# Optimization experiments

Hardware: AMD Instinct MI355X
Metric: run time of the kernel (lower is better)

## Reference

```python
import jax, jax.numpy as jnp
import numpy as np

N_NODES = 50000
N_EDGES = 800000
N_GRAPHS = 64
IN_DIM, HID, MLP_HID, NUM_CLASSES = 384, 128, 64, 1


def setup_inputs() -> dict:
    key = jax.random.key(0)
    ks = jax.random.split(key, 10)
    x = jax.random.normal(ks[0], (N_NODES, IN_DIM), jnp.float32)
    edge_index = jax.random.randint(ks[1], (2, N_EDGES), 0, N_NODES, dtype=jnp.int32)
    batch = jnp.sort(jax.random.randint(ks[2], (N_NODES,), 0, N_GRAPHS, dtype=jnp.int32))

    def glorot(k, shape):
        fan_in = shape[0]
        return jax.random.normal(k, shape, jnp.float32) / jnp.sqrt(jnp.float32(fan_in))

    return {
        "x": x,
        "edge_index": edge_index,
        "batch": batch,
        "W1": glorot(ks[3], (IN_DIM, HID)),  "b1": jnp.zeros((HID,), jnp.float32),
        "W2": glorot(ks[4], (HID, HID)),     "b2": jnp.zeros((HID,), jnp.float32),
        "W3": glorot(ks[5], (HID, HID)),     "b3": jnp.zeros((HID,), jnp.float32),
        "Wm1": glorot(ks[6], (HID, MLP_HID)), "bm1": jnp.zeros((MLP_HID,), jnp.float32),
        "Wm2": glorot(ks[7], (MLP_HID, NUM_CLASSES)), "bm2": jnp.zeros((NUM_CLASSES,), jnp.float32),
    }


def _gcn_conv(x, W, b, src, dst, dis):
    # PyG GCNConv: h = x W; aggregate D^-1/2 (A+I) D^-1/2 h; add bias.
    n = x.shape[0]
    h = x @ W                               # [N, out]
    enorm = dis[src] * dis[dst]             # [E] symmetric normalization
    msgs = h[src] * enorm[:, None]          # gather + scale
    agg = jax.ops.segment_sum(msgs, dst, num_segments=n)
    agg = agg + h * (dis * dis)[:, None]    # self-loop contribution
    return agg + b


def reference(x, edge_index, batch, W1, b1, W2, b2, W3, b3, Wm1, bm1, Wm2, bm2):
    src, dst = edge_index[0], edge_index[1]
    n = x.shape[0]
    # degree over A + I (self-loops added, as in PyG gcn_norm)
    deg = jax.ops.segment_sum(jnp.ones((src.shape[0],), x.dtype), dst, num_segments=n) + 1.0
    dis = jax.lax.rsqrt(deg)

    h = jax.nn.relu(_gcn_conv(x, W1, b1, src, dst, dis))
    h = jax.nn.relu(_gcn_conv(h, W2, b2, src, dst, dis))
    h = jax.nn.relu(_gcn_conv(h, W3, b3, src, dst, dis))

    # global mean pool over graphs
    counts = jax.ops.segment_sum(jnp.ones((n,), x.dtype), batch, num_segments=N_GRAPHS)
    pooled = jax.ops.segment_sum(h, batch, num_segments=N_GRAPHS)
    pooled = pooled / jnp.maximum(counts, 1.0)[:, None]   # [G, HID]

    # MLP head (dropout = identity in eval mode)
    z = jax.nn.relu(pooled @ Wm1 + bm1)
    out = z @ Wm2 + bm2                                    # [G, 1]
    return out
```

## Files before the change

kernel.cpp:

```cpp
#include <hip/hip_runtime.h>
#include <hip/hip_bf16.h>

#define N_NODES 50000
#define N_EDGES 800000
#define N_GRAPHS 64
#define IN_DIM 384
#define HID 128
#define MLP_HID 64

#define SCAN_BLOCKS ((N_NODES + 255) / 256)
#define POOL_CHUNK 128
#define POOL_BLOCKS ((N_NODES + POOL_CHUNK - 1) / POOL_CHUNK)
#define GEMM_BLOCKS ((N_NODES + 127) / 128)

typedef __attribute__((ext_vector_type(8))) short short8;
typedef __attribute__((ext_vector_type(4))) float f32x4;
typedef unsigned int u32;

__global__ __launch_bounds__(256) void count_kernel(const int* __restrict__ dst,
                                                    int* __restrict__ cnt, int E) {
    int t = blockIdx.x * 256 + threadIdx.x;
    if (t < E) atomicAdd(&cnt[dst[t]], 1);
}

__global__ __launch_bounds__(256) void bsum_kernel(const int* __restrict__ cnt,
                                                   int* __restrict__ bsum) {
    __shared__ int sh[256];
    const int t = threadIdx.x;
    const int i = blockIdx.x * 256 + t;
    sh[t] = (i < N_NODES) ? cnt[i] : 0;
    __syncthreads();
#pragma unroll
    for (int off = 128; off > 0; off >>= 1) {
        if (t < off) sh[t] += sh[t + off];
        __syncthreads();
    }
    if (t == 0) bsum[blockIdx.x] = sh[0];
}

__global__ __launch_bounds__(256) void bscan_kernel(const int* __restrict__ bsum,
                                                    int* __restrict__ boff,
                                                    int* __restrict__ rowptr) {
    __shared__ int sh[256];
    const int t = threadIdx.x;
    int v = (t < SCAN_BLOCKS) ? bsum[t] : 0;
    sh[t] = v;
    __syncthreads();
#pragma unroll
    for (int off = 1; off < 256; off <<= 1) {
        int u = 0;
        if (t >= off) u = sh[t - off];
        __syncthreads();
        if (t >= off) sh[t] += u;
        __syncthreads();
    }
    if (t < SCAN_BLOCKS) boff[t] = sh[t] - v;
    if (t == 255) rowptr[N_NODES] = sh[255];
}

__global__ __launch_bounds__(256) void final_scan_kernel(const int* __restrict__ cnt,
                                                         const int* __restrict__ boff,
                                                         int* __restrict__ rowptr,
                                                         int* __restrict__ cursor,
                                                         float* __restrict__ dis) {
    __shared__ int sh[256];
    const int t = threadIdx.x;
    const int i = blockIdx.x * 256 + t;
    const int c = (i < N_NODES) ? cnt[i] : 0;
    sh[t] = c;
    __syncthreads();
#pragma unroll
    for (int off = 1; off < 256; off <<= 1) {
        int u = 0;
        if (t >= off) u = sh[t - off];
        __syncthreads();
        if (t >= off) sh[t] += u;
        __syncthreads();
    }
    if (i < N_NODES) {
        const int pos = boff[blockIdx.x] + sh[t] - c;
        rowptr[i] = pos;
        cursor[i] = pos;
        dis[i] = rsqrtf((float)c + 1.0f);
    }
}

__global__ __launch_bounds__(256) void fill_kernel(const int* __restrict__ ei,
                                                   int* __restrict__ cursor,
                                                   int* __restrict__ csr, int E) {
    int e = blockIdx.x * 256 + threadIdx.x;
    if (e >= E) return;
    int s = ei[e];
    int d = ei[E + e];
    int pos = atomicAdd(&cursor[d], 1);
    csr[pos] = s;
}

__global__ __launch_bounds__(256) void wsplit_kernel(const float* __restrict__ W,
                                                     ushort* __restrict__ hi,
                                                     ushort* __restrict__ lo, int K) {
    int t = blockIdx.x * 256 + threadIdx.x;
    if (t >= K * 128) return;
    const int k = t >> 7;
    const int c = t & 127;
    const float f = W[t];
    const u32 u = __float_as_uint(f);
    const u32 h = u & 0xFFFF0000u;
    const float lf = f - __uint_as_float(h);
    hi[c * K + k] = (ushort)(u >> 16);
    lo[c * K + k] = (ushort)(__float_as_uint(lf) >> 16);
}

template <int K, bool RELU_IN>
__global__ __launch_bounds__(256) void gemm_mfma_kernel(const float* __restrict__ X,
                                                        const ushort* __restrict__ Wthi,
                                                        const ushort* __restrict__ Wtlo,
                                                        float* __restrict__ H, int M) {
    __shared__ ushort Ahi[128][40];
    __shared__ ushort Alo[128][40];
    __shared__ ushort Bhi[128][40];
    __shared__ ushort Blo[128][40];

    const int tid = threadIdx.x;
    const int row0 = blockIdx.x * 128;

    const int srow = tid >> 1;
    const int skq  = (tid & 1) << 4;

    const int lane = tid & 63;
    const int wave = tid >> 6;
    const int wr = (wave >> 1) * 64;
    const int wc = (wave & 1) * 64;
    const int li = lane & 15;
    const int kb = (lane >> 4) << 3;

    f32x4 acc[4][4];
#pragma unroll
    for (int m = 0; m < 4; ++m)
#pragma unroll
        for (int n = 0; n < 4; ++n) acc[m][n] = (f32x4){0.f, 0.f, 0.f, 0.f};

    for (int k0 = 0; k0 < K; k0 += 32) {
        {
            const int gr = row0 + srow;
            const float* src = &X[(size_t)(gr < M ? gr : (M - 1)) * K + k0 + skq];
            float f[16];
            *reinterpret_cast<float4*>(f)      = *reinterpret_cast<const float4*>(src);
            *reinterpret_cast<float4*>(f + 4)  = *reinterpret_cast<const float4*>(src + 4);
            *reinterpret_cast<float4*>(f + 8)  = *reinterpret_cast<const float4*>(src + 8);
            *reinterpret_cast<float4*>(f + 12) = *reinterpret_cast<const float4*>(src + 12);
            u32 hp[8], lp[8];
#pragma unroll
            for (int i = 0; i < 8; ++i) {
                float f0 = f[2 * i], f1 = f[2 * i + 1];
                if (RELU_IN) { f0 = fmaxf(f0, 0.f); f1 = fmaxf(f1, 0.f); }
                const u32 u0 = __float_as_uint(f0), u1 = __float_as_uint(f1);
                const u32 h0 = u0 & 0xFFFF0000u, h1 = u1 & 0xFFFF0000u;
                const float l0 = f0 - __uint_as_float(h0);
                const float l1 = f1 - __uint_as_float(h1);
                hp[i] = (h0 >> 16) | h1;
                lp[i] = (__float_as_uint(l0) >> 16) | (__float_as_uint(l1) & 0xFFFF0000u);
            }
            u32* dh = (u32*)&Ahi[srow][skq];
            u32* dl = (u32*)&Alo[srow][skq];
            *reinterpret_cast<uint4*>(dh)     = make_uint4(hp[0], hp[1], hp[2], hp[3]);
            *reinterpret_cast<uint4*>(dh + 4) = make_uint4(hp[4], hp[5], hp[6], hp[7]);
            *reinterpret_cast<uint4*>(dl)     = make_uint4(lp[0], lp[1], lp[2], lp[3]);
            *reinterpret_cast<uint4*>(dl + 4) = make_uint4(lp[4], lp[5], lp[6], lp[7]);
        }
        {
            const ushort* sh = &Wthi[srow * K + k0 + skq];
            const ushort* sl = &Wtlo[srow * K + k0 + skq];
            *reinterpret_cast<uint4*>(&Bhi[srow][skq])     = *reinterpret_cast<const uint4*>(sh);
            *reinterpret_cast<uint4*>(&Bhi[srow][skq + 8]) = *reinterpret_cast<const uint4*>(sh + 8);
            *reinterpret_cast<uint4*>(&Blo[srow][skq])     = *reinterpret_cast<const uint4*>(sl);
            *reinterpret_cast<uint4*>(&Blo[srow][skq + 8]) = *reinterpret_cast<const uint4*>(sl + 8);
        }
        __syncthreads();
        short8 ah[4], al[4];
#pragma unroll
        for (int m = 0; m < 4; ++m) {
            ah[m] = *reinterpret_cast<const short8*>(&Ahi[wr + m * 16 + li][kb]);
            al[m] = *reinterpret_cast<const short8*>(&Alo[wr + m * 16 + li][kb]);
        }
#pragma unroll
        for (int n = 0; n < 4; ++n) {
            const short8 bh = *reinterpret_cast<const short8*>(&Bhi[wc + n * 16 + li][kb]);
            const short8 bl = *reinterpret_cast<const short8*>(&Blo[wc + n * 16 + li][kb]);
#pragma unroll
            for (int m = 0; m < 4; ++m) {
                acc[m][n] = __builtin_amdgcn_mfma_f32_16x16x32_bf16(ah[m], bh, acc[m][n], 0, 0, 0);
                acc[m][n] = __builtin_amdgcn_mfma_f32_16x16x32_bf16(ah[m], bl, acc[m][n], 0, 0, 0);
                acc[m][n] = __builtin_amdgcn_mfma_f32_16x16x32_bf16(al[m], bh, acc[m][n], 0, 0, 0);
            }
        }
        __syncthreads();
    }
    const int rbase = (lane >> 4) << 2;
#pragma unroll
    for (int m = 0; m < 4; ++m) {
        const int gr0 = row0 + wr + m * 16 + rbase;
#pragma unroll
        for (int r = 0; r < 4; ++r) {
            const int grow = gr0 + r;
            if (grow < M) {
#pragma unroll
                for (int n = 0; n < 4; ++n) {
                    H[(size_t)grow * 128 + wc + n * 16 + li] = acc[m][n][r];
                }
            }
        }
    }
}

__global__ __launch_bounds__(256) void gather_kernel(const int* __restrict__ rowptr,
                                                     const int* __restrict__ csr,
                                                     const float* __restrict__ H,
                                                     const float* __restrict__ dis,
                                                     const float* __restrict__ b,
                                                     float* __restrict__ AGG, int n) {
    int t = blockIdx.x * 256 + threadIdx.x;
    int node = t >> 5;
    if (node >= n) return;
    int lane = t & 31;
    const int beg = rowptr[node];
    const int end = rowptr[node + 1];
    const float d = dis[node];

    float4 acc;
    {
        float4 h = *reinterpret_cast<const float4*>(&H[node * 128 + lane * 4]);
        float4 bb = *reinterpret_cast<const float4*>(&b[lane * 4]);
        const float dd = d * d;
        acc.x = fmaf(h.x, dd, bb.x);
        acc.y = fmaf(h.y, dd, bb.y);
        acc.z = fmaf(h.z, dd, bb.z);
        acc.w = fmaf(h.w, dd, bb.w);
    }
    int i = beg;
    for (; i + 2 <= end; i += 2) {
        const int s0 = csr[i];
        const int s1 = csr[i + 1];
        const float e0 = dis[s0] * d;
        const float e1 = dis[s1] * d;
        float4 v0 = *reinterpret_cast<const float4*>(&H[s0 * 128 + lane * 4]);
        float4 v1 = *reinterpret_cast<const float4*>(&H[s1 * 128 + lane * 4]);
        acc.x = fmaf(v0.x, e0, acc.x);
        acc.y = fmaf(v0.y, e0, acc.y);
        acc.z = fmaf(v0.z, e0, acc.z);
        acc.w = fmaf(v0.w, e0, acc.w);
        acc.x = fmaf(v1.x, e1, acc.x);
        acc.y = fmaf(v1.y, e1, acc.y);
        acc.z = fmaf(v1.z, e1, acc.z);
        acc.w = fmaf(v1.w, e1, acc.w);
    }
    if (i < end) {
        const int s0 = csr[i];
        const float e0 = dis[s0] * d;
        float4 v0 = *reinterpret_cast<const float4*>(&H[s0 * 128 + lane * 4]);
        acc.x = fmaf(v0.x, e0, acc.x);
        acc.y = fmaf(v0.y, e0, acc.y);
        acc.z = fmaf(v0.z, e0, acc.z);
        acc.w = fmaf(v0.w, e0, acc.w);
    }
    *reinterpret_cast<float4*>(&AGG[node * 128 + lane * 4]) = acc;
}

__global__ __launch_bounds__(256) void pool1_kernel(const float* __restrict__ AGG,
                                                    const int* __restrict__ batch,
                                                    float* __restrict__ pooled, int n) {
    const int start = blockIdx.x * POOL_CHUNK;
    const int end = min(start + POOL_CHUNK, n);
    const int f = threadIdx.x & 127;
    const int h = threadIdx.x >> 7;
    int gcur = -1;
    float acc = 0.f;
    for (int i = start + h; i < end; i += 2) {
        const int g = batch[i];
        if (g != gcur) {
            if (gcur >= 0) atomicAdd(&pooled[gcur * HID + f], acc);
            gcur = g;
            acc = 0.f;
        }
        acc += fmaxf(AGG[i * HID + f], 0.f);
    }
    if (gcur >= 0) atomicAdd(&pooled[gcur * HID + f], acc);
}

__global__ __launch_bounds__(128) void pooldiv_kernel(const int* __restrict__ batch,
                                                      float* __restrict__ pooled, int n) {
    const int g = blockIdx.x;
    int lo = 0, hi = n;
    while (lo < hi) { int mid = (lo + hi) >> 1; if (batch[mid] < g) lo = mid + 1; else hi = mid; }
    const int start = lo;
    hi = n;
    while (lo < hi) { int mid = (lo + hi) >> 1; if (batch[mid] < g + 1) lo = mid + 1; else hi = mid; }
    const float cnt = (float)(lo - start);
    pooled[g * HID + threadIdx.x] /= fmaxf(cnt, 1.f);
}

__global__ __launch_bounds__(256) void mlp_kernel(const float* __restrict__ pooled,
                                                  const float* __restrict__ Wm1,
                                                  const float* __restrict__ bm1,
                                                  const float* __restrict__ Wm2,
                                                  const float* __restrict__ bm2,
                                                  float* __restrict__ out) {
    __shared__ float P[N_GRAPHS][HID];
    __shared__ float Wl[HID][MLP_HID];
    const int tid = threadIdx.x;
    for (int i = tid; i < N_GRAPHS * HID; i += 256) P[i >> 7][i & 127] = pooled[i];
    for (int i = tid; i < HID * MLP_HID; i += 256) Wl[i >> 6][i & 63] = Wm1[i];
    __syncthreads();
    const int g = tid >> 2;
    const int jb = tid & 3;
    float part = 0.f;
#pragma unroll
    for (int jj = 0; jj < 16; ++jj) {
        const int j = jb * 16 + jj;
        float z = bm1[j];
        for (int k = 0; k < HID; ++k) z = fmaf(P[g][k], Wl[k][j], z);
        z = fmaxf(z, 0.f);
        part = fmaf(z, Wm2[j], part);
    }
    part += __shfl_xor(part, 1);
    part += __shfl_xor(part, 2);
    if (jb == 0) out[g] = part + bm2[0];
}

extern "C" void kernel_launch(void* const* d_in, const int* in_sizes, int n_in,
                              void* d_out, int out_size, void* d_ws, size_t ws_size,
                              hipStream_t stream) {
    const float* x   = (const float*)d_in[0];
    const int*   ei  = (const int*)d_in[1];
    const int*   bat = (const int*)d_in[2];
    const float* W1  = (const float*)d_in[3];
    const float* b1  = (const float*)d_in[4];
    const float* W2  = (const float*)d_in[5];
    const float* b2  = (const float*)d_in[6];
    const float* W3  = (const float*)d_in[7];
    const float* b3  = (const float*)d_in[8];
    const float* Wm1 = (const float*)d_in[9];
    const float* bm1 = (const float*)d_in[10];
    const float* Wm2 = (const float*)d_in[11];
    const float* bm2 = (const float*)d_in[12];
    float* out = (float*)d_out;

    int*   cnt    = (int*)d_ws;
    int*   cursor = cnt + 50048;
    int*   rowptr = cursor + 50048;
    int*   csr    = rowptr + 50056;
    int*   bsum   = csr + 800000;
    int*   boff   = bsum + 256;
    float* dis    = (float*)(boff + 256);
    float* H      = dis + 50048;
    float* AGG    = H + N_NODES * HID;
    float* pooled = AGG + N_NODES * HID;
    ushort* wt1hi = (ushort*)(pooled + 8192);
    ushort* wt1lo = wt1hi + IN_DIM * HID;
    ushort* wt2hi = wt1lo + IN_DIM * HID;
    ushort* wt2lo = wt2hi + HID * HID;
    ushort* wt3hi = wt2lo + HID * HID;
    ushort* wt3lo = wt3hi + HID * HID;

    hipMemsetAsync(cnt, 0, N_NODES * sizeof(int), stream);
    hipMemsetAsync(pooled, 0, N_GRAPHS * HID * sizeof(float), stream);

    count_kernel<<<(N_EDGES + 255) / 256, 256, 0, stream>>>(ei + N_EDGES, cnt, N_EDGES);
    bsum_kernel<<<SCAN_BLOCKS, 256, 0, stream>>>(cnt, bsum);
    bscan_kernel<<<1, 256, 0, stream>>>(bsum, boff, rowptr);
    final_scan_kernel<<<SCAN_BLOCKS, 256, 0, stream>>>(cnt, boff, rowptr, cursor, dis);
    fill_kernel<<<(N_EDGES + 255) / 256, 256, 0, stream>>>(ei, cursor, csr, N_EDGES);

    wsplit_kernel<<<(IN_DIM * HID + 255) / 256, 256, 0, stream>>>(W1, wt1hi, wt1lo, IN_DIM);
    wsplit_kernel<<<(HID * HID + 255) / 256, 256, 0, stream>>>(W2, wt2hi, wt2lo, HID);
    wsplit_kernel<<<(HID * HID + 255) / 256, 256, 0, stream>>>(W3, wt3hi, wt3lo, HID);

    const int gat_blocks = (N_NODES * 32 + 255) / 256;

    gemm_mfma_kernel<IN_DIM, false><<<GEMM_BLOCKS, 256, 0, stream>>>(x, wt1hi, wt1lo, H, N_NODES);
    gather_kernel<<<gat_blocks, 256, 0, stream>>>(rowptr, csr, H, dis, b1, AGG, N_NODES);
    gemm_mfma_kernel<HID, true><<<GEMM_BLOCKS, 256, 0, stream>>>(AGG, wt2hi, wt2lo, H, N_NODES);
    gather_kernel<<<gat_blocks, 256, 0, stream>>>(rowptr, csr, H, dis, b2, AGG, N_NODES);
    gemm_mfma_kernel<HID, true><<<GEMM_BLOCKS, 256, 0, stream>>>(AGG, W3 ? wt3hi : wt3hi, wt3lo, H, N_NODES);
    gather_kernel<<<gat_blocks, 256, 0, stream>>>(rowptr, csr, H, dis, b3, AGG, N_NODES);

    pool1_kernel<<<POOL_BLOCKS, 256, 0, stream>>>(AGG, bat, pooled, N_NODES);
    pooldiv_kernel<<<N_GRAPHS, 128, 0, stream>>>(bat, pooled, N_NODES);
    mlp_kernel<<<1, 256, 0, stream>>>(pooled, Wm1, bm1, Wm2, bm2, out);
}
```

Baseline: 537.7 us.

## Pre-scale GEMM output by dis, simplify gather, fuse pooling, merge wsplits

The GEMM epilogue now multiplies each output row by its dis value. This lets the gather drop the per-edge dis[src] load and its multiply and apply the destination scale once at the end. The gather switches to one 64-lane wavefront per node with float2 loads and 4-way unrolling. The last layer's gather fuses ReLU and mean-pool accumulation through shared memory and atomics, which removes the separate pool kernel and one full pass over AGG. The three weight-split launches are merged into one kernel; the cost is an extra dis load in the GEMM and more atomics when a block spans graph boundaries.

```diff
diff --git a/kernel.cpp b/kernel.cpp
--- a/kernel.cpp
+++ b/kernel.cpp
@@ -9,9 +9,8 @@
 #define MLP_HID 64
 
 #define SCAN_BLOCKS ((N_NODES + 255) / 256)
-#define POOL_CHUNK 128
-#define POOL_BLOCKS ((N_NODES + POOL_CHUNK - 1) / POOL_CHUNK)
 #define GEMM_BLOCKS ((N_NODES + 127) / 128)
+#define GATHER_BLOCKS (N_NODES / 4)
 
 typedef __attribute__((ext_vector_type(8))) short short8;
 typedef __attribute__((ext_vector_type(4))) float f32x4;
@@ -96,11 +95,8 @@
     csr[pos] = s;
 }
 
-__global__ __launch_bounds__(256) void wsplit_kernel(const float* __restrict__ W,
-                                                     ushort* __restrict__ hi,
-                                                     ushort* __restrict__ lo, int K) {
-    int t = blockIdx.x * 256 + threadIdx.x;
-    if (t >= K * 128) return;
+__device__ __forceinline__ void wsplit_one(const float* W, ushort* hi, ushort* lo,
+                                           int K, int t) {
     const int k = t >> 7;
     const int c = t & 127;
     const float f = W[t];
@@ -111,11 +107,26 @@
     lo[c * K + k] = (ushort)(__float_as_uint(lf) >> 16);
 }
 
+__global__ __launch_bounds__(256) void wsplit_kernel(const float* __restrict__ W1,
+                                                     const float* __restrict__ W2,
+                                                     const float* __restrict__ W3,
+                                                     ushort* __restrict__ w1hi, ushort* __restrict__ w1lo,
+                                                     ushort* __restrict__ w2hi, ushort* __restrict__ w2lo,
+                                                     ushort* __restrict__ w3hi, ushort* __restrict__ w3lo) {
+    int t = blockIdx.x * 256 + threadIdx.x;
+    if (t < IN_DIM * HID) wsplit_one(W1, w1hi, w1lo, IN_DIM, t);
+    if (t < HID * HID) {
+        wsplit_one(W2, w2hi, w2lo, HID, t);
+        wsplit_one(W3, w3hi, w3lo, HID, t);
+    }
+}
+
 template <int K, bool RELU_IN>
 __global__ __launch_bounds__(256) void gemm_mfma_kernel(const float* __restrict__ X,
                                                         const ushort* __restrict__ Wthi,
                                                         const ushort* __restrict__ Wtlo,
-                                                        float* __restrict__ H, int M) {
+                                                        const float* __restrict__ dis,
+                                                        float* __restrict__ Hs, int M) {
     __shared__ ushort Ahi[128][40];
     __shared__ ushort Alo[128][40];
     __shared__ ushort Bhi[128][40];
@@ -204,87 +215,77 @@
         for (int r = 0; r < 4; ++r) {
             const int grow = gr0 + r;
             if (grow < M) {
+                const float dv = dis[grow];
 #pragma unroll
                 for (int n = 0; n < 4; ++n) {
-                    H[(size_t)grow * 128 + wc + n * 16 + li] = acc[m][n][r];
+                    Hs[(size_t)grow * 128 + wc + n * 16 + li] = acc[m][n][r] * dv;
                 }
             }
         }
     }
 }
 
+template <bool POOL>
 __global__ __launch_bounds__(256) void gather_kernel(const int* __restrict__ rowptr,
                                                      const int* __restrict__ csr,
-                                                     const float* __restrict__ H,
+                                                     const float* __restrict__ Hs,
                                                      const float* __restrict__ dis,
                                                      const float* __restrict__ b,
-                                                     float* __restrict__ AGG, int n) {
-    int t = blockIdx.x * 256 + threadIdx.x;
-    int node = t >> 5;
-    if (node >= n) return;
-    int lane = t & 31;
+                                                     float* __restrict__ AGG,
+                                                     const int* __restrict__ batch,
+                                                     float* __restrict__ pooled) {
+    const int wave = threadIdx.x >> 6;
+    const int lane = threadIdx.x & 63;
+    const int node = blockIdx.x * 4 + wave;
+    const int f2 = lane * 2;
     const int beg = rowptr[node];
     const int end = rowptr[node + 1];
+
+    float2 acc = *reinterpret_cast<const float2*>(&Hs[(size_t)node * 128 + f2]);
+    int i = beg;
+    for (; i + 4 <= end; i += 4) {
+        const int s0 = csr[i], s1 = csr[i + 1], s2 = csr[i + 2], s3 = csr[i + 3];
+        const float2 v0 = *reinterpret_cast<const float2*>(&Hs[(size_t)s0 * 128 + f2]);
+        const float2 v1 = *reinterpret_cast<const float2*>(&Hs[(size_t)s1 * 128 + f2]);
+        const float2 v2 = *reinterpret_cast<const float2*>(&Hs[(size_t)s2 * 128 + f2]);
+        const float2 v3 = *reinterpret_cast<const float2*>(&Hs[(size_t)s3 * 128 + f2]);
+        acc.x += (v0.x + v1.x) + (v2.x + v3.x);
+        acc.y += (v0.y + v1.y) + (v2.y + v3.y);
+    }
+    for (; i < end; ++i) {
+        const int s = csr[i];
+        const float2 v = *reinterpret_cast<const float2*>(&Hs[(size_t)s * 128 + f2]);
+        acc.x += v.x;
+        acc.y += v.y;
+    }
     const float d = dis[node];
-
-    float4 acc;
-    {
-        float4 h = *reinterpret_cast<const float4*>(&H[node * 128 + lane * 4]);
-        float4 bb = *reinterpret_cast<const float4*>(&b[lane * 4]);
-        const float dd = d * d;
-        acc.x = fmaf(h.x, dd, bb.x);
-        acc.y = fmaf(h.y, dd, bb.y);
-        acc.z = fmaf(h.z, dd, bb.z);
-        acc.w = fmaf(h.w, dd, bb.w);
-    }
-    int i = beg;
-    for (; i + 2 <= end; i += 2) {
-        const int s0 = csr[i];
-        const int s1 = csr[i + 1];
-        const float e0 = dis[s0] * d;
-        const float e1 = dis[s1] * d;
-        float4 v0 = *reinterpret_cast<const float4*>(&H[s0 * 128 + lane * 4]);
-        float4 v1 = *reinterpret_cast<const float4*>(&H[s1 * 128 + lane * 4]);
-        acc.x = fmaf(v0.x, e0, acc.x);
-        acc.y = fmaf(v0.y, e0, acc.y);
-        acc.z = fmaf(v0.z, e0, acc.z);
-        acc.w = fmaf(v0.w, e0, acc.w);
-        acc.x = fmaf(v1.x, e1, acc.x);
-        acc.y = fmaf(v1.y, e1, acc.y);
-        acc.z = fmaf(v1.z, e1, acc.z);
-        acc.w = fmaf(v1.w, e1, acc.w);
-    }
-    if (i < end) {
-        const int s0 = csr[i];
-        const float e0 = dis[s0] * d;
-        float4 v0 = *reinterpret_cast<const float4*>(&H[s0 * 128 + lane * 4]);
-        acc.x = fmaf(v0.x, e0, acc.x);
-        acc.y = fmaf(v0.y, e0, acc.y);
-        acc.z = fmaf(v0.z, e0, acc.z);
-        acc.w = fmaf(v0.w, e0, acc.w);
-    }
-    *reinterpret_cast<float4*>(&AGG[node * 128 + lane * 4]) = acc;
-}
-
-__global__ __launch_bounds__(256) void pool1_kernel(const float* __restrict__ AGG,
-                                                    const int* __restrict__ batch,
-                                                    float* __restrict__ pooled, int n) {
-    const int start = blockIdx.x * POOL_CHUNK;
-    const int end = min(start + POOL_CHUNK, n);
-    const int f = threadIdx.x & 127;
-    const int h = threadIdx.x >> 7;
-    int gcur = -1;
-    float acc = 0.f;
-    for (int i = start + h; i < end; i += 2) {
-        const int g = batch[i];
-        if (g != gcur) {
-            if (gcur >= 0) atomicAdd(&pooled[gcur * HID + f], acc);
-            gcur = g;
-            acc = 0.f;
-        }
-        acc += fmaxf(AGG[i * HID + f], 0.f);
-    }
-    if (gcur >= 0) atomicAdd(&pooled[gcur * HID + f], acc);
+    float2 o;
+    o.x = fmaf(acc.x, d, b[f2]);
+    o.y = fmaf(acc.y, d, b[f2 + 1]);
+
+    if (!POOL) {
+        *reinterpret_cast<float2*>(&AGG[(size_t)node * 128 + f2]) = o;
+    } else {
+        o.x = fmaxf(o.x, 0.f);
+        o.y = fmaxf(o.y, 0.f);
+        __shared__ float part[4][128];
+        __shared__ int gs[4];
+        const int g = batch[node];
+        if (lane == 0) gs[wave] = g;
+        part[wave][f2] = o.x;
+        part[wave][f2 + 1] = o.y;
+        __syncthreads();
+        if (gs[0] == gs[1] && gs[1] == gs[2] && gs[2] == gs[3]) {
+            if (threadIdx.x < 128) {
+                const float s = (part[0][threadIdx.x] + part[1][threadIdx.x]) +
+                                (part[2][threadIdx.x] + part[3][threadIdx.x]);
+                atomicAdd(&pooled[gs[0] * HID + threadIdx.x], s);
+            }
+        } else {
+            atomicAdd(&pooled[g * HID + f2], o.x);
+            atomicAdd(&pooled[g * HID + f2 + 1], o.y);
+        }
+    }
 }
 
 __global__ __launch_bounds__(128) void pooldiv_kernel(const int* __restrict__ batch,
@@ -371,20 +372,16 @@
     final_scan_kernel<<<SCAN_BLOCKS, 256, 0, stream>>>(cnt, boff, rowptr, cursor, dis);
     fill_kernel<<<(N_EDGES + 255) / 256, 256, 0, stream>>>(ei, cursor, csr, N_EDGES);
 
-    wsplit_kernel<<<(IN_DIM * HID + 255) / 256, 256, 0, stream>>>(W1, wt1hi, wt1lo, IN_DIM);
-    wsplit_kernel<<<(HID * HID + 255) / 256, 256, 0, stream>>>(W2, wt2hi, wt2lo, HID);
-    wsplit_kernel<<<(HID * HID + 255) / 256, 256, 0, stream>>>(W3, wt3hi, wt3lo, HID);
-
-    const int gat_blocks = (N_NODES * 32 + 255) / 256;
-
-    gemm_mfma_kernel<IN_DIM, false><<<GEMM_BLOCKS, 256, 0, stream>>>(x, wt1hi, wt1lo, H, N_NODES);
-    gather_kernel<<<gat_blocks, 256, 0, stream>>>(rowptr, csr, H, dis, b1, AGG, N_NODES);
-    gemm_mfma_kernel<HID, true><<<GEMM_BLOCKS, 256, 0, stream>>>(AGG, wt2hi, wt2lo, H, N_NODES);
-    gather_kernel<<<gat_blocks, 256, 0, stream>>>(rowptr, csr, H, dis, b2, AGG, N_NODES);
-    gemm_mfma_kernel<HID, true><<<GEMM_BLOCKS, 256, 0, stream>>>(AGG, W3 ? wt3hi : wt3hi, wt3lo, H, N_NODES);
-    gather_kernel<<<gat_blocks, 256, 0, stream>>>(rowptr, csr, H, dis, b3, AGG, N_NODES);
-
-    pool1_kernel<<<POOL_BLOCKS, 256, 0, stream>>>(AGG, bat, pooled, N_NODES);
+    wsplit_kernel<<<(IN_DIM * HID + 255) / 256, 256, 0, stream>>>(
+        W1, W2, W3, wt1hi, wt1lo, wt2hi, wt2lo, wt3hi, wt3lo);
+
+    gemm_mfma_kernel<IN_DIM, false><<<GEMM_BLOCKS, 256, 0, stream>>>(x, wt1hi, wt1lo, dis, H, N_NODES);
+    gather_kernel<false><<<GATHER_BLOCKS, 256, 0, stream>>>(rowptr, csr, H, dis, b1, AGG, bat, pooled);
+    gemm_mfma_kernel<HID, true><<<GEMM_BLOCKS, 256, 0, stream>>>(AGG, wt2hi, wt2lo, dis, H, N_NODES);
+    gather_kernel<false><<<GATHER_BLOCKS, 256, 0, stream>>>(rowptr, csr, H, dis, b2, AGG, bat, pooled);
+    gemm_mfma_kernel<HID, true><<<GEMM_BLOCKS, 256, 0, stream>>>(AGG, wt3hi, wt3lo, dis, H, N_NODES);
+    gather_kernel<true><<<GATHER_BLOCKS, 256, 0, stream>>>(rowptr, csr, H, dis, b3, AGG, bat, pooled);
+
     pooldiv_kernel<<<N_GRAPHS, 128, 0, stream>>>(bat, pooled, N_NODES);
     mlp_kernel<<<1, 256, 0, stream>>>(pooled, Wm1, bm1, Wm2, bm2, out);
 }
```

Measured after the change: 522.8 us. -2.8%, faster.
